# Performance work log

Measured on AMD Instinct MI355X. Metric: run time of the kernel, lower is better.

The kernel has to match this reference:

```python
import jax, jax.numpy as jnp
import numpy as np

N_NODES = 50000
N_EDGES = 800000
IN_CH = 384
HID = 128


def _gcn_conv(x, src, dst, W, b, n):
    # PyG GCNConv: h = x @ W; out[dst] += d^-1/2[src] * d^-1/2[dst] * h[src]; out += b
    h = x @ W  # [N, out_ch]
    deg = jax.ops.segment_sum(jnp.ones(src.shape, dtype=h.dtype), dst, num_segments=n)
    dinv = jnp.where(deg > 0, jax.lax.rsqrt(jnp.maximum(deg, 1.0)), 0.0)
    norm = dinv[src] * dinv[dst]  # [E]
    out = jax.ops.segment_sum(h[src] * norm[:, None], dst, num_segments=n)
    return out + b


def setup_inputs() -> dict:
    key = jax.random.key(0)
    k_x, k_e, k1, k2, k3, k4 = jax.random.split(key, 6)
    x = jax.random.normal(k_x, (N_NODES, IN_CH), dtype=jnp.float32)
    edge_index = jax.random.randint(k_e, (2, N_EDGES), 0, N_NODES, dtype=jnp.int64)
    s1 = 1.0 / np.sqrt(IN_CH)
    s2 = 1.0 / np.sqrt(HID)
    W1 = jax.random.uniform(k1, (IN_CH, HID), jnp.float32, -s1, s1)
    b1 = jnp.zeros((HID,), jnp.float32)
    W2 = jax.random.uniform(k2, (HID, HID), jnp.float32, -s2, s2)
    b2 = jnp.zeros((HID,), jnp.float32)
    return {"x": x, "edge_index": edge_index, "W1": W1, "b1": b1, "W2": W2, "b2": b2}


def reference(x, edge_index, W1, b1, W2, b2):
    n = x.shape[0]
    loops = jnp.arange(n, dtype=edge_index.dtype)
    src = jnp.concatenate([edge_index[0], loops])  # add_self_loops
    dst = jnp.concatenate([edge_index[1], loops])
    h = _gcn_conv(x, src, dst, W1, b1, n)
    h = jax.nn.relu(h)  # dropout is identity in eval mode
    out = _gcn_conv(h, src, dst, W2, b2, n)
    return out
```

## Files before the change

### kernel.cpp

```cpp
#include <hip/hip_runtime.h>
#include <hip/hip_fp16.h>

#define NN 50000
#define NE 800000
#define C_IN 384
#define C_HID 128
#define NB 196
#define CHK 128
#define ECH 6250
#define NBKT 128
#define BSTR 392

typedef __attribute__((ext_vector_type(8))) short short8;
typedef __attribute__((ext_vector_type(4))) float f32x4;
typedef __attribute__((ext_vector_type(4))) unsigned short us4;

__device__ __forceinline__ ushort f2bf(float x) {
    uint u = __float_as_uint(x);
    uint r = (u + 0x7fffu + ((u >> 16) & 1u)) >> 16;
    return (ushort)r;
}
__device__ __forceinline__ float bf2f(ushort b) { return __uint_as_float(((uint)b) << 16); }

typedef __attribute__((address_space(1))) const unsigned int as1_uint;
typedef __attribute__((address_space(3))) unsigned int as3_uint;
__device__ __forceinline__ void gload16(const void* g, void* l) {
    __builtin_amdgcn_global_load_lds((as1_uint*)g, (as3_uint*)l, 16, 0, 0);
}

__global__ __launch_bounds__(256) void k_dinv(const int* __restrict__ cnt,
                                              float* __restrict__ dinv) {
    int i = blockIdx.x * 256 + threadIdx.x;
    if (i < NN) dinv[i] = rsqrtf((float)cnt[i] + 1.0f);
}

__global__ __launch_bounds__(256) void k_bsum(const int* __restrict__ cnt,
                                              int* __restrict__ bsum) {
    __shared__ int part[256];
    const int tid = threadIdx.x;
    const int i = blockIdx.x * 256 + tid;
    part[tid] = (i < NN) ? cnt[i] : 0;
    __syncthreads();
#pragma unroll
    for (int off = 128; off > 0; off >>= 1) {
        if (tid < off) part[tid] += part[tid + off];
        __syncthreads();
    }
    if (tid == 0) bsum[blockIdx.x] = part[0];
}

__global__ __launch_bounds__(256) void k_sbs(const int* __restrict__ bsum,
                                             int* __restrict__ bpre) {
    __shared__ int part[256];
    const int t = threadIdx.x;
    part[t] = (t < NB) ? bsum[t] : 0;
    __syncthreads();
#pragma unroll
    for (int off = 1; off < 256; off <<= 1) {
        int v = (t >= off) ? part[t - off] : 0;
        __syncthreads();
        part[t] += v;
        __syncthreads();
    }
    if (t < NB) bpre[t] = (t == 0) ? 0 : part[t - 1];
}

__global__ __launch_bounds__(256) void k_write(const int* __restrict__ cnt,
                                               const int* __restrict__ bpre,
                                               int* __restrict__ rowptr) {
    __shared__ int part[256];
    const int t = threadIdx.x;
    const int i = blockIdx.x * 256 + t;
    const int v = (i < NN) ? cnt[i] : 0;
    part[t] = v;
    __syncthreads();
#pragma unroll
    for (int off = 1; off < 256; off <<= 1) {
        int u = (t >= off) ? part[t - off] : 0;
        __syncthreads();
        part[t] += u;
        __syncthreads();
    }
    if (i < NN) {
        const int excl = bpre[blockIdx.x] + part[t] - v;
        rowptr[i] = excl;
        if (i == NN - 1) rowptr[NN] = excl + v;
    }
}

__global__ __launch_bounds__(256) void k_hist(const int* __restrict__ dst,
                                              int* __restrict__ histT) {
    __shared__ int h[NBKT];
    const int tid = threadIdx.x;
    if (tid < NBKT) h[tid] = 0;
    __syncthreads();
    const int base = blockIdx.x * ECH;
    for (int i = base + tid; i < base + ECH; i += 256)
        atomicAdd(&h[(uint)dst[i] / BSTR], 1);
    __syncthreads();
    if (tid < NBKT) histT[tid * CHK + blockIdx.x] = h[tid];
}

__global__ __launch_bounds__(1024) void k_hscan(const int* __restrict__ histT,
                                                int* __restrict__ histS) {
    __shared__ int part[1024];
    const int t = threadIdx.x;
    const int base = t * 16;
    int loc[16];
    int s = 0;
#pragma unroll
    for (int i = 0; i < 16; ++i) {
        loc[i] = histT[base + i];
        s += loc[i];
    }
    part[t] = s;
    __syncthreads();
    for (int off = 1; off < 1024; off <<= 1) {
        int v = (t >= off) ? part[t - off] : 0;
        __syncthreads();
        part[t] += v;
        __syncthreads();
    }
    int run = (t == 0) ? 0 : part[t - 1];
#pragma unroll
    for (int i = 0; i < 16; ++i) {
        histS[base + i] = run;
        run += loc[i];
    }
}

__global__ __launch_bounds__(256) void k_binscat(const int* __restrict__ src,
                                                 const int* __restrict__ dst,
                                                 const int* __restrict__ histS,
                                                 uint2* __restrict__ mid) {
    __shared__ int cur[NBKT];
    const int tid = threadIdx.x;
    if (tid < NBKT) cur[tid] = histS[tid * CHK + blockIdx.x];
    __syncthreads();
    const int base = blockIdx.x * ECH;
    for (int i = base + tid; i < base + ECH; i += 256) {
        const int s = src[i];
        const int d = dst[i];
        const int p = atomicAdd(&cur[(uint)d / BSTR], 1);
        mid[p] = make_uint2((uint)d, (uint)s << 16);
    }
}

__global__ __launch_bounds__(256) void k_bcnt(const uint2* __restrict__ mid,
                                              const int* __restrict__ histS,
                                              int* __restrict__ cnt) {
    __shared__ int cur[BSTR];
    const int tid = threadIdx.x;
    const int b = blockIdx.x;
    for (int j = tid; j < BSTR; j += 256) cur[j] = 0;
    __syncthreads();
    const int lo = histS[b * CHK];
    const int hi = (b < NBKT - 1) ? histS[(b + 1) * CHK] : NE;
    for (int e = lo + tid; e < hi; e += 256)
        atomicAdd(&cur[mid[e].x - (uint)b * BSTR], 1);
    __syncthreads();
    for (int j = tid; j < BSTR; j += 256) {
        const int idx = b * BSTR + j;
        if (idx < NN) cnt[idx] = cur[j];
    }
}

__global__ __launch_bounds__(256) void k_binfill(const uint2* __restrict__ mid,
                                                 const int* __restrict__ histS,
                                                 const int* __restrict__ rowptr,
                                                 const float* __restrict__ dinv,
                                                 uint* __restrict__ csr) {
    __shared__ int cur[BSTR];
    __shared__ float sdv[BSTR];
    const int tid = threadIdx.x;
    const int b = blockIdx.x;
    for (int j = tid; j < BSTR; j += 256) {
        const int idx = b * BSTR + j;
        cur[j] = (idx < NN) ? rowptr[idx] : 0;
        sdv[j] = (idx < NN) ? dinv[idx] : 0.f;
    }
    __syncthreads();
    const int lo = histS[b * CHK];
    const int hi = (b < NBKT - 1) ? histS[(b + 1) * CHK] : NE;
    for (int e = lo + tid; e < hi; e += 256) {
        const uint2 u = mid[e];
        const int j = u.x - (uint)b * BSTR;
        const float norm = dinv[u.y >> 16] * sdv[j];
        const int p = atomicAdd(&cur[j], 1);
        csr[p] = u.y | __half_as_ushort(__float2half(norm));
    }
}

__global__ __launch_bounds__(256) void k_wconv(const float* __restrict__ W,
                                               ushort* __restrict__ Wt,
                                               int K) {
    int i = blockIdx.x * 256 + threadIdx.x;
    if (i < K * C_HID) {
        int k = i >> 7, n = i & 127;
        float w = W[i];
        ushort h = f2bf(w);
        ushort l = f2bf(w - bf2f(h));
        int blk = k >> 5, kq = (k >> 3) & 3, j = k & 7;
        int t = n >> 4, fr = n & 15, lane = kq * 16 + fr;
        size_t off = ((size_t)blk * 1024 + t * 64 + lane) * 8 + j;
        Wt[off] = h;
        Wt[off + 4096] = l;
    }
}

#define STAGE_X(NXT, XOLD, KB1)                                                          \
    {                                                                                    \
        float xs0 = XOLD.x, xs1 = XOLD.y, xs2 = XOLD.z, xs3 = XOLD.w;                    \
        if (IN_RELU_BIAS) {                                                              \
            float4 bq = *(const float4*)(&bias_lds[(KB1) * 32 + (tid & 7) * 4]);         \
            xs0 = fmaxf(xs0 + bq.x, 0.f);                                                \
            xs1 = fmaxf(xs1 + bq.y, 0.f);                                                \
            xs2 = fmaxf(xs2 + bq.z, 0.f);                                                \
            xs3 = fmaxf(xs3 + bq.w, 0.f);                                                \
        }                                                                                \
        const uint u0 = __float_as_uint(xs0), u1 = __float_as_uint(xs1);                 \
        const uint u2 = __float_as_uint(xs2), u3 = __float_as_uint(xs3);                 \
        const uint h01 = (u0 >> 16) | (u1 & 0xffff0000u);                                \
        const uint h23 = (u2 >> 16) | (u3 & 0xffff0000u);                                \
        const uint l0 = __float_as_uint(xs0 - __uint_as_float(u0 & 0xffff0000u));        \
        const uint l1 = __float_as_uint(xs1 - __uint_as_float(u1 & 0xffff0000u));        \
        const uint l2 = __float_as_uint(xs2 - __uint_as_float(u2 & 0xffff0000u));        \
        const uint l3 = __float_as_uint(xs3 - __uint_as_float(u3 & 0xffff0000u));        \
        const uint l01 = (l0 >> 16) | (l1 & 0xffff0000u);                                \
        const uint l23 = (l2 >> 16) | (l3 & 0xffff0000u);                                \
        *(uint2*)&XLh[NXT][xw] = make_uint2(h01, h23);                                   \
        *(uint2*)&XLl[NXT][xw] = make_uint2(l01, l23);                                   \
    }

#define GEMM_BODY(KB, CUR, NXT, XOLD, XNEW)                                              \
    {                                                                                    \
        _Pragma("unroll")                                                                \
        for (int i_ = 0; i_ < 2; ++i_)                                                   \
            gload16(Wt8 + (size_t)((KB) + 1) * 1024 + wv * 128 + i_ * 64 + lane,         \
                    &WL[NXT][wv * 128 + i_ * 64]);                                       \
        __builtin_amdgcn_sched_barrier(0);                                               \
        XNEW = *(const float4*)(xsrc + ((KB) + 2) * 32);                                 \
        const short8 ahh = *(const short8*)&XLh[CUR][axh];                               \
        const short8 all = *(const short8*)&XLl[CUR][axh];                               \
        const short8 wh0 = WL[CUR][(tb + 0) * 64 + lane];                                \
        const short8 wl0 = WL[CUR][512 + (tb + 0) * 64 + lane];                          \
        const short8 wh1 = WL[CUR][(tb + 1) * 64 + lane];                                \
        const short8 wl1 = WL[CUR][512 + (tb + 1) * 64 + lane];                          \
        const short8 wh2 = WL[CUR][(tb + 2) * 64 + lane];                                \
        const short8 wl2 = WL[CUR][512 + (tb + 2) * 64 + lane];                          \
        const short8 wh3 = WL[CUR][(tb + 3) * 64 + lane];                                \
        const short8 wl3 = WL[CUR][512 + (tb + 3) * 64 + lane];                          \
        STAGE_X(NXT, XOLD, (KB) + 1);                                                    \
        __builtin_amdgcn_s_setprio(1);                                                   \
        acc[0] = __builtin_amdgcn_mfma_f32_16x16x32_bf16(ahh, wh0, acc[0], 0, 0, 0);     \
        acc[0] = __builtin_amdgcn_mfma_f32_16x16x32_bf16(ahh, wl0, acc[0], 0, 0, 0);     \
        acc[0] = __builtin_amdgcn_mfma_f32_16x16x32_bf16(all, wh0, acc[0], 0, 0, 0);     \
        acc[1] = __builtin_amdgcn_mfma_f32_16x16x32_bf16(ahh, wh1, acc[1], 0, 0, 0);     \
        acc[1] = __builtin_amdgcn_mfma_f32_16x16x32_bf16(ahh, wl1, acc[1], 0, 0, 0);     \
        acc[1] = __builtin_amdgcn_mfma_f32_16x16x32_bf16(all, wh1, acc[1], 0, 0, 0);     \
        acc[2] = __builtin_amdgcn_mfma_f32_16x16x32_bf16(ahh, wh2, acc[2], 0, 0, 0);     \
        acc[2] = __builtin_amdgcn_mfma_f32_16x16x32_bf16(ahh, wl2, acc[2], 0, 0, 0);     \
        acc[2] = __builtin_amdgcn_mfma_f32_16x16x32_bf16(all, wh2, acc[2], 0, 0, 0);     \
        acc[3] = __builtin_amdgcn_mfma_f32_16x16x32_bf16(ahh, wh3, acc[3], 0, 0, 0);     \
        acc[3] = __builtin_amdgcn_mfma_f32_16x16x32_bf16(ahh, wl3, acc[3], 0, 0, 0);     \
        acc[3] = __builtin_amdgcn_mfma_f32_16x16x32_bf16(all, wh3, acc[3], 0, 0, 0);     \
        __builtin_amdgcn_s_setprio(0);                                                   \
        __builtin_amdgcn_sched_barrier(0);                                               \
        asm volatile("s_waitcnt vmcnt(1) lgkmcnt(0)" ::: "memory");                      \
        __builtin_amdgcn_sched_barrier(0);                                               \
        __builtin_amdgcn_s_barrier();                                                    \
    }

#define GEMM_TAIL(KB, CUR, DO_MFMA_ONLY)                                                 \
    {                                                                                    \
        const short8 ahh = *(const short8*)&XLh[CUR][axh];                               \
        const short8 all = *(const short8*)&XLl[CUR][axh];                               \
        const short8 wh0 = WL[CUR][(tb + 0) * 64 + lane];                                \
        const short8 wl0 = WL[CUR][512 + (tb + 0) * 64 + lane];                          \
        const short8 wh1 = WL[CUR][(tb + 1) * 64 + lane];                                \
        const short8 wl1 = WL[CUR][512 + (tb + 1) * 64 + lane];                          \
        const short8 wh2 = WL[CUR][(tb + 2) * 64 + lane];                                \
        const short8 wl2 = WL[CUR][512 + (tb + 2) * 64 + lane];                          \
        const short8 wh3 = WL[CUR][(tb + 3) * 64 + lane];                                \
        const short8 wl3 = WL[CUR][512 + (tb + 3) * 64 + lane];                          \
        acc[0] = __builtin_amdgcn_mfma_f32_16x16x32_bf16(ahh, wh0, acc[0], 0, 0, 0);     \
        acc[0] = __builtin_amdgcn_mfma_f32_16x16x32_bf16(ahh, wl0, acc[0], 0, 0, 0);     \
        acc[0] = __builtin_amdgcn_mfma_f32_16x16x32_bf16(all, wh0, acc[0], 0, 0, 0);     \
        acc[1] = __builtin_amdgcn_mfma_f32_16x16x32_bf16(ahh, wh1, acc[1], 0, 0, 0);     \
        acc[1] = __builtin_amdgcn_mfma_f32_16x16x32_bf16(ahh, wl1, acc[1], 0, 0, 0);     \
        acc[1] = __builtin_amdgcn_mfma_f32_16x16x32_bf16(all, wh1, acc[1], 0, 0, 0);     \
        acc[2] = __builtin_amdgcn_mfma_f32_16x16x32_bf16(ahh, wh2, acc[2], 0, 0, 0);     \
        acc[2] = __builtin_amdgcn_mfma_f32_16x16x32_bf16(ahh, wl2, acc[2], 0, 0, 0);     \
        acc[2] = __builtin_amdgcn_mfma_f32_16x16x32_bf16(all, wh2, acc[2], 0, 0, 0);     \
        acc[3] = __builtin_amdgcn_mfma_f32_16x16x32_bf16(ahh, wh3, acc[3], 0, 0, 0);     \
        acc[3] = __builtin_amdgcn_mfma_f32_16x16x32_bf16(ahh, wl3, acc[3], 0, 0, 0);     \
        acc[3] = __builtin_amdgcn_mfma_f32_16x16x32_bf16(all, wh3, acc[3], 0, 0, 0);     \
    }

template <bool IN_RELU_BIAS, bool OUT_BIAS>
__global__ __launch_bounds__(512) void k_gemm_mfma(const float* __restrict__ X,
                                                   const ushort* __restrict__ Wt,
                                                   const float* __restrict__ bin,
                                                   const float* __restrict__ bout,
                                                   const float* __restrict__ dinv,
                                                   ushort* __restrict__ out_main,
                                                   float* __restrict__ out_self,
                                                   int K) {
    __shared__ short8 WL[2][1024];
    __shared__ ushort XLh[2][2048];
    __shared__ ushort XLl[2][2048];
    __shared__ float bias_lds[128];

    const int tid = threadIdx.x;
    const int bm = blockIdx.x * 64;
    const int wv = tid >> 6;
    const int lane = tid & 63;
    const int fr = lane & 15;
    const int kq = lane >> 4;
    const int g = wv >> 1;
    const int ch = wv & 1;
    const int tb = ch * 4;
    const int NK = K >> 5;

    const short8* Wt8 = (const short8*)Wt;

    const int xr = tid >> 3;
    const int xc8 = tid & 7;
    int xrow = bm + xr;
    if (xrow >= NN) xrow = NN - 1;
    const float* xsrc = X + (size_t)xrow * K + xc8 * 4;
    const int xw = xr * 32 + (((xc8 >> 1) ^ (xr & 3)) << 3) + ((xc8 & 1) << 2);

    const int ar = g * 16 + fr;
    const int axh = ar * 32 + ((kq ^ (ar & 3)) << 3);

    f32x4 acc[4];
#pragma unroll
    for (int t = 0; t < 4; ++t) acc[t] = (f32x4){0.f, 0.f, 0.f, 0.f};

    if (IN_RELU_BIAS && tid < 128) bias_lds[tid] = bin[tid];

#pragma unroll
    for (int i_ = 0; i_ < 2; ++i_)
        gload16(Wt8 + (size_t)wv * 128 + i_ * 64 + lane, &WL[0][wv * 128 + i_ * 64]);
    __builtin_amdgcn_sched_barrier(0);
    float4 xA = *(const float4*)(xsrc);
    float4 xB = *(const float4*)(xsrc + 32);
    asm volatile("s_waitcnt lgkmcnt(0)" ::: "memory");
    __builtin_amdgcn_s_barrier();
    STAGE_X(0, xA, 0);
    xA = xB;
    asm volatile("s_waitcnt lgkmcnt(0)" ::: "memory");
    __builtin_amdgcn_s_barrier();

    for (int kb = 0; kb < NK - 2; kb += 2) {
        GEMM_BODY(kb, 0, 1, xA, xB);
        GEMM_BODY(kb + 1, 1, 0, xB, xA);
    }

    {
        const int KB = NK - 2;
#pragma unroll
        for (int i_ = 0; i_ < 2; ++i_)
            gload16(Wt8 + (size_t)(KB + 1) * 1024 + wv * 128 + i_ * 64 + lane,
                    &WL[1][wv * 128 + i_ * 64]);
        STAGE_X(1, xA, KB + 1);
        GEMM_TAIL(KB, 0, 0);
        __builtin_amdgcn_sched_barrier(0);
        asm volatile("s_waitcnt vmcnt(0) lgkmcnt(0)" ::: "memory");
        __builtin_amdgcn_sched_barrier(0);
        __builtin_amdgcn_s_barrier();
    }
    GEMM_TAIL(NK - 1, 1, 1);

#pragma unroll
    for (int r = 0; r < 4; ++r) {
        const int m = bm + g * 16 + kq * 4 + r;
        if (m < NN) {
            const float dv = dinv[m];
            const float d2 = dv * dv;
            ushort* om = out_main + (size_t)m * C_HID;
            float* os = out_self + (size_t)m * C_HID;
#pragma unroll
            for (int t = 0; t < 4; ++t) {
                const int n = (ch * 4 + t) * 16 + fr;
                const float v = acc[t][r];
                om[n] = f2bf(v);
                os[n] = v * d2 + (OUT_BIAS ? bout[n] : 0.f);
            }
        }
    }
}

__global__ __launch_bounds__(256) void k_gather(const ushort* __restrict__ h,
                                                const int* __restrict__ rowptr,
                                                const uint* __restrict__ csr,
                                                float* __restrict__ out) {
    const int tid = threadIdx.x;
    const int node = blockIdx.x * 8 + (tid >> 5);
    if (node >= NN) return;
    const int lane = tid & 31;
    const int c = lane * 4;
    const int beg = rowptr[node];
    const int end = rowptr[node + 1];

    float4 acc = *(const float4*)(out + (size_t)node * C_HID + c);

    for (int j0 = beg; j0 < end; j0 += 32) {
        const int n = end - j0;
        uint myE = 0;
        if (lane < n) myE = csr[j0 + lane];
        const int m = n < 32 ? n : 32;
        int jj = 0;
        for (; jj + 4 <= m; jj += 4) {
            const uint e0 = (uint)__shfl((int)myE, jj + 0, 32);
            const uint e1 = (uint)__shfl((int)myE, jj + 1, 32);
            const uint e2 = (uint)__shfl((int)myE, jj + 2, 32);
            const uint e3 = (uint)__shfl((int)myE, jj + 3, 32);
            const us4 u0 = *(const us4*)(h + (size_t)(e0 >> 16) * C_HID + c);
            const us4 u1 = *(const us4*)(h + (size_t)(e1 >> 16) * C_HID + c);
            const us4 u2 = *(const us4*)(h + (size_t)(e2 >> 16) * C_HID + c);
            const us4 u3 = *(const us4*)(h + (size_t)(e3 >> 16) * C_HID + c);
            const float n0 = __half2float(__ushort_as_half((ushort)(e0 & 0xffffu)));
            const float n1 = __half2float(__ushort_as_half((ushort)(e1 & 0xffffu)));
            const float n2 = __half2float(__ushort_as_half((ushort)(e2 & 0xffffu)));
            const float n3 = __half2float(__ushort_as_half((ushort)(e3 & 0xffffu)));
            acc.x = fmaf(bf2f(u0[0]), n0, acc.x);
            acc.y = fmaf(bf2f(u0[1]), n0, acc.y);
            acc.z = fmaf(bf2f(u0[2]), n0, acc.z);
            acc.w = fmaf(bf2f(u0[3]), n0, acc.w);
            acc.x = fmaf(bf2f(u1[0]), n1, acc.x);
            acc.y = fmaf(bf2f(u1[1]), n1, acc.y);
            acc.z = fmaf(bf2f(u1[2]), n1, acc.z);
            acc.w = fmaf(bf2f(u1[3]), n1, acc.w);
            acc.x = fmaf(bf2f(u2[0]), n2, acc.x);
            acc.y = fmaf(bf2f(u2[1]), n2, acc.y);
            acc.z = fmaf(bf2f(u2[2]), n2, acc.z);
            acc.w = fmaf(bf2f(u2[3]), n2, acc.w);
            acc.x = fmaf(bf2f(u3[0]), n3, acc.x);
            acc.y = fmaf(bf2f(u3[1]), n3, acc.y);
            acc.z = fmaf(bf2f(u3[2]), n3, acc.z);
            acc.w = fmaf(bf2f(u3[3]), n3, acc.w);
        }
        for (; jj < m; ++jj) {
            const uint ev = (uint)__shfl((int)myE, jj, 32);
            const us4 u = *(const us4*)(h + (size_t)(ev >> 16) * C_HID + c);
            const float nw = __half2float(__ushort_as_half((ushort)(ev & 0xffffu)));
            acc.x = fmaf(bf2f(u[0]), nw, acc.x);
            acc.y = fmaf(bf2f(u[1]), nw, acc.y);
            acc.z = fmaf(bf2f(u[2]), nw, acc.z);
            acc.w = fmaf(bf2f(u[3]), nw, acc.w);
        }
    }
    *(float4*)(out + (size_t)node * C_HID + c) = acc;
}

extern "C" void kernel_launch(void* const* d_in, const int* in_sizes, int n_in,
                              void* d_out, int out_size, void* d_ws, size_t ws_size,
                              hipStream_t stream) {
    const float* x = (const float*)d_in[0];
    const int* ei = (const int*)d_in[1];
    const float* W1 = (const float*)d_in[2];
    const float* b1 = (const float*)d_in[3];
    const float* W2 = (const float*)d_in[4];
    const float* b2 = (const float*)d_in[5];
    float* out = (float*)d_out;

    const int* src = ei;
    const int* dst = ei + NE;

    int* cnt = (int*)d_ws;
    int* rowptr = cnt + 50048;
    float* dinv = (float*)(rowptr + 50064);
    int* bsum = (int*)(dinv + 50048);
    int* bpre = bsum + 256;
    int* histT = bpre + 256;
    int* histS = histT + 16384;
    ushort* Wt1 = (ushort*)(histS + 16384);
    ushort* Wt2 = Wt1 + 98304;
    uint* csr = (uint*)(Wt2 + 32768);
    uint2* mid = (uint2*)(csr + NE);
    ushort* A_bf = (ushort*)(mid + NE);
    float* B = (float*)(A_bf + (size_t)NN * C_HID);

    k_wconv<<<(C_IN * C_HID + 255) / 256, 256, 0, stream>>>(W1, Wt1, C_IN);
    k_wconv<<<(C_HID * C_HID + 255) / 256, 256, 0, stream>>>(W2, Wt2, C_HID);
    k_hist<<<CHK, 256, 0, stream>>>(dst, histT);
    k_hscan<<<1, 1024, 0, stream>>>(histT, histS);
    k_binscat<<<CHK, 256, 0, stream>>>(src, dst, histS, mid);
    k_bcnt<<<NBKT, 256, 0, stream>>>(mid, histS, cnt);
    k_dinv<<<NB, 256, 0, stream>>>(cnt, dinv);
    k_bsum<<<NB, 256, 0, stream>>>(cnt, bsum);
    k_sbs<<<1, 256, 0, stream>>>(bsum, bpre);
    k_write<<<NB, 256, 0, stream>>>(cnt, bpre, rowptr);
    k_binfill<<<NBKT, 256, 0, stream>>>(mid, histS, rowptr, dinv, csr);

    const int gblocks = (NN + 63) / 64;
    const int agblocks = (NN + 7) / 8;
    k_gemm_mfma<false, false><<<gblocks, 512, 0, stream>>>(x, Wt1, nullptr, nullptr, dinv, A_bf, B, C_IN);
    k_gather<<<agblocks, 256, 0, stream>>>(A_bf, rowptr, csr, B);
    k_gemm_mfma<true, true><<<gblocks, 512, 0, stream>>>(B, Wt2, b1, b2, dinv, A_bf, out, C_HID);
    k_gather<<<agblocks, 256, 0, stream>>>(A_bf, rowptr, csr, out);
}
```

Before: 300.7 us.

## Fuse CSR count/scan/dinv kernels, merge weight conversion, widen gather to 16 lanes

Merges the per-bucket degree count with a local prefix scan that writes rowptr and dinv directly, using the bucket offset from histS. This removes four kernels (dinv, bsum, sbs, write). The two weight-conversion launches are combined into one. The gather kernel now gives each node 16 lanes, each loading 8 bf16 values (16 bytes) per neighbor, so one block covers twice as many nodes. The aim is fewer launches and wider memory loads, at the cost of fewer lanes fetching edges in parallel per node.

```diff
diff --git a/kernel.cpp b/kernel.cpp
--- a/kernel.cpp
+++ b/kernel.cpp
@@ -5,7 +5,6 @@
 #define NE 800000
 #define C_IN 384
 #define C_HID 128
-#define NB 196
 #define CHK 128
 #define ECH 6250
 #define NBKT 128
@@ -13,7 +12,7 @@
 
 typedef __attribute__((ext_vector_type(8))) short short8;
 typedef __attribute__((ext_vector_type(4))) float f32x4;
-typedef __attribute__((ext_vector_type(4))) unsigned short us4;
+typedef __attribute__((ext_vector_type(8))) unsigned short us8;
 
 __device__ __forceinline__ ushort f2bf(float x) {
     uint u = __float_as_uint(x);
@@ -26,66 +25,6 @@
 typedef __attribute__((address_space(3))) unsigned int as3_uint;
 __device__ __forceinline__ void gload16(const void* g, void* l) {
     __builtin_amdgcn_global_load_lds((as1_uint*)g, (as3_uint*)l, 16, 0, 0);
-}
-
-__global__ __launch_bounds__(256) void k_dinv(const int* __restrict__ cnt,
-                                              float* __restrict__ dinv) {
-    int i = blockIdx.x * 256 + threadIdx.x;
-    if (i < NN) dinv[i] = rsqrtf((float)cnt[i] + 1.0f);
-}
-
-__global__ __launch_bounds__(256) void k_bsum(const int* __restrict__ cnt,
-                                              int* __restrict__ bsum) {
-    __shared__ int part[256];
-    const int tid = threadIdx.x;
-    const int i = blockIdx.x * 256 + tid;
-    part[tid] = (i < NN) ? cnt[i] : 0;
-    __syncthreads();
-#pragma unroll
-    for (int off = 128; off > 0; off >>= 1) {
-        if (tid < off) part[tid] += part[tid + off];
-        __syncthreads();
-    }
-    if (tid == 0) bsum[blockIdx.x] = part[0];
-}
-
-__global__ __launch_bounds__(256) void k_sbs(const int* __restrict__ bsum,
-                                             int* __restrict__ bpre) {
-    __shared__ int part[256];
-    const int t = threadIdx.x;
-    part[t] = (t < NB) ? bsum[t] : 0;
-    __syncthreads();
-#pragma unroll
-    for (int off = 1; off < 256; off <<= 1) {
-        int v = (t >= off) ? part[t - off] : 0;
-        __syncthreads();
-        part[t] += v;
-        __syncthreads();
-    }
-    if (t < NB) bpre[t] = (t == 0) ? 0 : part[t - 1];
-}
-
-__global__ __launch_bounds__(256) void k_write(const int* __restrict__ cnt,
-                                               const int* __restrict__ bpre,
-                                               int* __restrict__ rowptr) {
-    __shared__ int part[256];
-    const int t = threadIdx.x;
-    const int i = blockIdx.x * 256 + t;
-    const int v = (i < NN) ? cnt[i] : 0;
-    part[t] = v;
-    __syncthreads();
-#pragma unroll
-    for (int off = 1; off < 256; off <<= 1) {
-        int u = (t >= off) ? part[t - off] : 0;
-        __syncthreads();
-        part[t] += u;
-        __syncthreads();
-    }
-    if (i < NN) {
-        const int excl = bpre[blockIdx.x] + part[t] - v;
-        rowptr[i] = excl;
-        if (i == NN - 1) rowptr[NN] = excl + v;
-    }
 }
 
 __global__ __launch_bounds__(256) void k_hist(const int* __restrict__ dst,
@@ -146,10 +85,12 @@
     }
 }
 
-__global__ __launch_bounds__(256) void k_bcnt(const uint2* __restrict__ mid,
-                                              const int* __restrict__ histS,
-                                              int* __restrict__ cnt) {
+__global__ __launch_bounds__(256) void k_bcnt_scan(const uint2* __restrict__ mid,
+                                                   const int* __restrict__ histS,
+                                                   int* __restrict__ rowptr,
+                                                   float* __restrict__ dinv) {
     __shared__ int cur[BSTR];
+    __shared__ int part[256];
     const int tid = threadIdx.x;
     const int b = blockIdx.x;
     for (int j = tid; j < BSTR; j += 256) cur[j] = 0;
@@ -159,10 +100,28 @@
     for (int e = lo + tid; e < hi; e += 256)
         atomicAdd(&cur[mid[e].x - (uint)b * BSTR], 1);
     __syncthreads();
-    for (int j = tid; j < BSTR; j += 256) {
-        const int idx = b * BSTR + j;
-        if (idx < NN) cnt[idx] = cur[j];
-    }
+    const int i0 = 2 * tid;
+    const int v0 = (i0 < BSTR) ? cur[i0] : 0;
+    const int v1 = (i0 + 1 < BSTR) ? cur[i0 + 1] : 0;
+    part[tid] = v0 + v1;
+    __syncthreads();
+    for (int off = 1; off < 256; off <<= 1) {
+        int v = (tid >= off) ? part[tid - off] : 0;
+        __syncthreads();
+        part[tid] += v;
+        __syncthreads();
+    }
+    const int base = lo + ((tid > 0) ? part[tid - 1] : 0);
+    const int idx0 = b * BSTR + i0;
+    if (i0 < BSTR && idx0 < NN) {
+        rowptr[idx0] = base;
+        dinv[idx0] = rsqrtf((float)v0 + 1.0f);
+    }
+    if (i0 + 1 < BSTR && idx0 + 1 < NN) {
+        rowptr[idx0 + 1] = base + v0;
+        dinv[idx0 + 1] = rsqrtf((float)v1 + 1.0f);
+    }
+    if (b == NBKT - 1 && tid == 0) rowptr[NN] = NE;
 }
 
 __global__ __launch_bounds__(256) void k_binfill(const uint2* __restrict__ mid,
@@ -191,20 +150,28 @@
     }
 }
 
-__global__ __launch_bounds__(256) void k_wconv(const float* __restrict__ W,
-                                               ushort* __restrict__ Wt,
-                                               int K) {
+__device__ __forceinline__ void wconv_one(const float* W, ushort* Wt, int i) {
+    int k = i >> 7, n = i & 127;
+    float w = W[i];
+    ushort h = f2bf(w);
+    ushort l = f2bf(w - bf2f(h));
+    int blk = k >> 5, kq = (k >> 3) & 3, j = k & 7;
+    int t = n >> 4, fr = n & 15, lane = kq * 16 + fr;
+    size_t off = ((size_t)blk * 1024 + t * 64 + lane) * 8 + j;
+    Wt[off] = h;
+    Wt[off + 4096] = l;
+}
+
+__global__ __launch_bounds__(256) void k_wconv2(const float* __restrict__ W1,
+                                                const float* __restrict__ W2,
+                                                ushort* __restrict__ Wt1,
+                                                ushort* __restrict__ Wt2) {
     int i = blockIdx.x * 256 + threadIdx.x;
-    if (i < K * C_HID) {
-        int k = i >> 7, n = i & 127;
-        float w = W[i];
-        ushort h = f2bf(w);
-        ushort l = f2bf(w - bf2f(h));
-        int blk = k >> 5, kq = (k >> 3) & 3, j = k & 7;
-        int t = n >> 4, fr = n & 15, lane = kq * 16 + fr;
-        size_t off = ((size_t)blk * 1024 + t * 64 + lane) * 8 + j;
-        Wt[off] = h;
-        Wt[off + 4096] = l;
+    if (i < C_IN * C_HID) {
+        wconv_one(W1, Wt1, i);
+    } else {
+        int j = i - C_IN * C_HID;
+        if (j < C_HID * C_HID) wconv_one(W2, Wt2, j);
     }
 }
 
@@ -271,7 +238,7 @@
         __builtin_amdgcn_s_barrier();                                                    \
     }
 
-#define GEMM_TAIL(KB, CUR, DO_MFMA_ONLY)                                                 \
+#define GEMM_TAIL(CUR)                                                                   \
     {                                                                                    \
         const short8 ahh = *(const short8*)&XLh[CUR][axh];                               \
         const short8 all = *(const short8*)&XLl[CUR][axh];                               \
@@ -365,13 +332,13 @@
             gload16(Wt8 + (size_t)(KB + 1) * 1024 + wv * 128 + i_ * 64 + lane,
                     &WL[1][wv * 128 + i_ * 64]);
         STAGE_X(1, xA, KB + 1);
-        GEMM_TAIL(KB, 0, 0);
+        GEMM_TAIL(0);
         __builtin_amdgcn_sched_barrier(0);
         asm volatile("s_waitcnt vmcnt(0) lgkmcnt(0)" ::: "memory");
         __builtin_amdgcn_sched_barrier(0);
         __builtin_amdgcn_s_barrier();
     }
-    GEMM_TAIL(NK - 1, 1, 1);
+    GEMM_TAIL(1);
 
 #pragma unroll
     for (int r = 0; r < 4; ++r) {
@@ -397,62 +364,85 @@
                                                 const uint* __restrict__ csr,
                                                 float* __restrict__ out) {
     const int tid = threadIdx.x;
-    const int node = blockIdx.x * 8 + (tid >> 5);
+    const int node = blockIdx.x * 16 + (tid >> 4);
     if (node >= NN) return;
-    const int lane = tid & 31;
-    const int c = lane * 4;
+    const int lane = tid & 15;
+    const int c = lane * 8;
     const int beg = rowptr[node];
     const int end = rowptr[node + 1];
 
-    float4 acc = *(const float4*)(out + (size_t)node * C_HID + c);
-
-    for (int j0 = beg; j0 < end; j0 += 32) {
+    float* op = out + (size_t)node * C_HID + c;
+    float4 a0 = *(const float4*)(op);
+    float4 a1 = *(const float4*)(op + 4);
+
+    for (int j0 = beg; j0 < end; j0 += 16) {
         const int n = end - j0;
         uint myE = 0;
         if (lane < n) myE = csr[j0 + lane];
-        const int m = n < 32 ? n : 32;
+        const int m = n < 16 ? n : 16;
         int jj = 0;
         for (; jj + 4 <= m; jj += 4) {
-            const uint e0 = (uint)__shfl((int)myE, jj + 0, 32);
-            const uint e1 = (uint)__shfl((int)myE, jj + 1, 32);
-            const uint e2 = (uint)__shfl((int)myE, jj + 2, 32);
-            const uint e3 = (uint)__shfl((int)myE, jj + 3, 32);
-            const us4 u0 = *(const us4*)(h + (size_t)(e0 >> 16) * C_HID + c);
-            const us4 u1 = *(const us4*)(h + (size_t)(e1 >> 16) * C_HID + c);
-            const us4 u2 = *(const us4*)(h + (size_t)(e2 >> 16) * C_HID + c);
-            const us4 u3 = *(const us4*)(h + (size_t)(e3 >> 16) * C_HID + c);
+            const uint e0 = (uint)__shfl((int)myE, jj + 0, 16);
+            const uint e1 = (uint)__shfl((int)myE, jj + 1, 16);
+            const uint e2 = (uint)__shfl((int)myE, jj + 2, 16);
+            const uint e3 = (uint)__shfl((int)myE, jj + 3, 16);
+            const us8 u0 = *(const us8*)(h + (size_t)(e0 >> 16) * C_HID + c);
+            const us8 u1 = *(const us8*)(h + (size_t)(e1 >> 16) * C_HID + c);
+            const us8 u2 = *(const us8*)(h + (size_t)(e2 >> 16) * C_HID + c);
+            const us8 u3 = *(const us8*)(h + (size_t)(e3 >> 16) * C_HID + c);
             const float n0 = __half2float(__ushort_as_half((ushort)(e0 & 0xffffu)));
             const float n1 = __half2float(__ushort_as_half((ushort)(e1 & 0xffffu)));
             const float n2 = __half2float(__ushort_as_half((ushort)(e2 & 0xffffu)));
             const float n3 = __half2float(__ushort_as_half((ushort)(e3 & 0xffffu)));
-            acc.x = fmaf(bf2f(u0[0]), n0, acc.x);
-            acc.y = fmaf(bf2f(u0[1]), n0, acc.y);
-            acc.z = fmaf(bf2f(u0[2]), n0, acc.z);
-            acc.w = fmaf(bf2f(u0[3]), n0, acc.w);
-            acc.x = fmaf(bf2f(u1[0]), n1, acc.x);
-            acc.y = fmaf(bf2f(u1[1]), n1, acc.y);
-            acc.z = fmaf(bf2f(u1[2]), n1, acc.z);
-            acc.w = fmaf(bf2f(u1[3]), n1, acc.w);
-            acc.x = fmaf(bf2f(u2[0]), n2, acc.x);
-            acc.y = fmaf(bf2f(u2[1]), n2, acc.y);
-            acc.z = fmaf(bf2f(u2[2]), n2, acc.z);
-            acc.w = fmaf(bf2f(u2[3]), n2, acc.w);
-            acc.x = fmaf(bf2f(u3[0]), n3, acc.x);
-            acc.y = fmaf(bf2f(u3[1]), n3, acc.y);
-            acc.z = fmaf(bf2f(u3[2]), n3, acc.z);
-            acc.w = fmaf(bf2f(u3[3]), n3, acc.w);
+            a0.x = fmaf(bf2f(u0[0]), n0, a0.x);
+            a0.y = fmaf(bf2f(u0[1]), n0, a0.y);
+            a0.z = fmaf(bf2f(u0[2]), n0, a0.z);
+            a0.w = fmaf(bf2f(u0[3]), n0, a0.w);
+            a1.x = fmaf(bf2f(u0[4]), n0, a1.x);
+            a1.y = fmaf(bf2f(u0[5]), n0, a1.y);
+            a1.z = fmaf(bf2f(u0[6]), n0, a1.z);
+            a1.w = fmaf(bf2f(u0[7]), n0, a1.w);
+            a0.x = fmaf(bf2f(u1[0]), n1, a0.x);
+            a0.y = fmaf(bf2f(u1[1]), n1, a0.y);
+            a0.z = fmaf(bf2f(u1[2]), n1, a0.z);
+            a0.w = fmaf(bf2f(u1[3]), n1, a0.w);
+            a1.x = fmaf(bf2f(u1[4]), n1, a1.x);
+            a1.y = fmaf(bf2f(u1[5]), n1, a1.y);
+            a1.z = fmaf(bf2f(u1[6]), n1, a1.z);
+            a1.w = fmaf(bf2f(u1[7]), n1, a1.w);
+            a0.x = fmaf(bf2f(u2[0]), n2, a0.x);
+            a0.y = fmaf(bf2f(u2[1]), n2, a0.y);
+            a0.z = fmaf(bf2f(u2[2]), n2, a0.z);
+            a0.w = fmaf(bf2f(u2[3]), n2, a0.w);
+            a1.x = fmaf(bf2f(u2[4]), n2, a1.x);
+            a1.y = fmaf(bf2f(u2[5]), n2, a1.y);
+            a1.z = fmaf(bf2f(u2[6]), n2, a1.z);
+            a1.w = fmaf(bf2f(u2[7]), n2, a1.w);
+            a0.x = fmaf(bf2f(u3[0]), n3, a0.x);
+            a0.y = fmaf(bf2f(u3[1]), n3, a0.y);
+            a0.z = fmaf(bf2f(u3[2]), n3, a0.z);
+            a0.w = fmaf(bf2f(u3[3]), n3, a0.w);
+            a1.x = fmaf(bf2f(u3[4]), n3, a1.x);
+            a1.y = fmaf(bf2f(u3[5]), n3, a1.y);
+            a1.z = fmaf(bf2f(u3[6]), n3, a1.z);
+            a1.w = fmaf(bf2f(u3[7]), n3, a1.w);
         }
         for (; jj < m; ++jj) {
-            const uint ev = (uint)__shfl((int)myE, jj, 32);
-            const us4 u = *(const us4*)(h + (size_t)(ev >> 16) * C_HID + c);
+            const uint ev = (uint)__shfl((int)myE, jj, 16);
+            const us8 u = *(const us8*)(h + (size_t)(ev >> 16) * C_HID + c);
             const float nw = __half2float(__ushort_as_half((ushort)(ev & 0xffffu)));
-            acc.x = fmaf(bf2f(u[0]), nw, acc.x);
-            acc.y = fmaf(bf2f(u[1]), nw, acc.y);
-            acc.z = fmaf(bf2f(u[2]), nw, acc.z);
-            acc.w = fmaf(bf2f(u[3]), nw, acc.w);
+            a0.x = fmaf(bf2f(u[0]), nw, a0.x);
+            a0.y = fmaf(bf2f(u[1]), nw, a0.y);
+            a0.z = fmaf(bf2f(u[2]), nw, a0.z);
+            a0.w = fmaf(bf2f(u[3]), nw, a0.w);
+            a1.x = fmaf(bf2f(u[4]), nw, a1.x);
+            a1.y = fmaf(bf2f(u[5]), nw, a1.y);
+            a1.z = fmaf(bf2f(u[6]), nw, a1.z);
+            a1.w = fmaf(bf2f(u[7]), nw, a1.w);
         }
     }
-    *(float4*)(out + (size_t)node * C_HID + c) = acc;
+    *(float4*)(op) = a0;
+    *(float4*)(op + 4) = a1;
 }
 
 extern "C" void kernel_launch(void* const* d_in, const int* in_sizes, int n_in,
@@ -483,20 +473,15 @@
     ushort* A_bf = (ushort*)(mid + NE);
     float* B = (float*)(A_bf + (size_t)NN * C_HID);
 
-    k_wconv<<<(C_IN * C_HID + 255) / 256, 256, 0, stream>>>(W1, Wt1, C_IN);
-    k_wconv<<<(C_HID * C_HID + 255) / 256, 256, 0, stream>>>(W2, Wt2, C_HID);
+    k_wconv2<<<(C_IN * C_HID + C_HID * C_HID + 255) / 256, 256, 0, stream>>>(W1, W2, Wt1, Wt2);
     k_hist<<<CHK, 256, 0, stream>>>(dst, histT);
     k_hscan<<<1, 1024, 0, stream>>>(histT, histS);
     k_binscat<<<CHK, 256, 0, stream>>>(src, dst, histS, mid);
-    k_bcnt<<<NBKT, 256, 0, stream>>>(mid, histS, cnt);
-    k_dinv<<<NB, 256, 0, stream>>>(cnt, dinv);
-    k_bsum<<<NB, 256, 0, stream>>>(cnt, bsum);
-    k_sbs<<<1, 256, 0, stream>>>(bsum, bpre);
-    k_write<<<NB, 256, 0, stream>>>(cnt, bpre, rowptr);
+    k_bcnt_scan<<<NBKT, 256, 0, stream>>>(mid, histS, rowptr, dinv);
     k_binfill<<<NBKT, 256, 0, stream>>>(mid, histS, rowptr, dinv, csr);
 
     const int gblocks = (NN + 63) / 64;
-    const int agblocks = (NN + 7) / 8;
+    const int agblocks = (NN + 15) / 16;
     k_gemm_mfma<false, false><<<gblocks, 512, 0, stream>>>(x, Wt1, nullptr, nullptr, dinv, A_bf, B, C_IN);
     k_gather<<<agblocks, 256, 0, stream>>>(A_bf, rowptr, csr, B);
     k_gemm_mfma<true, true><<<gblocks, 512, 0, stream>>>(B, Wt2, b1, b2, dinv, A_bf, out, C_HID);
```

Measured after the change: 296.9 us. No clear change (-1.3%).
